# Kernel optimization log

Measured on AMD Instinct MI355X. Metric: run time of the kernel, lower is better.

Reference implementation:

```python
import jax, jax.numpy as jnp
import numpy as np

EMBED_DIM = 512
NUM_HEADS = 8
HEAD_DIM = EMBED_DIM // NUM_HEADS


def setup_inputs() -> dict:
    key = jax.random.key(0)
    ks = jax.random.split(key, 6)
    B, S, E = 2, 4096, EMBED_DIM
    scale = 1.0 / np.sqrt(E)
    return {
        "rotation_params": jax.random.normal(ks[0], (E, E), jnp.float32) * scale,
        "entangle_params": jax.random.normal(ks[1], (E, E), jnp.float32) * scale,
        "inputs": jax.random.normal(ks[2], (B, S, E), jnp.float32),
        "w_q": jax.random.normal(ks[3], (E, E), jnp.float32) * scale,
        "w_k": jax.random.normal(ks[4], (E, E), jnp.float32) * scale,
        "w_v": jax.random.normal(ks[5], (E, E), jnp.float32) * scale,
    }


def reference(rotation_params, entangle_params, inputs, w_q, w_k, w_v):
    B, S, E = inputs.shape
    H, D = NUM_HEADS, HEAD_DIM
    # torch nn.Linear(x) = x @ W.T ; then extra matmul with rotation/entangle mats
    q = (inputs @ w_q.T) @ rotation_params  # [B,S,E]
    k = (inputs @ w_k.T) @ entangle_params  # [B,S,E]
    v = inputs @ w_v.T                       # [B,S,E]
    # split heads -> [B,H,S,D]
    q = q.reshape(B, S, H, D).transpose(0, 2, 1, 3)
    k = k.reshape(B, S, H, D).transpose(0, 2, 1, 3)
    v = v.reshape(B, S, H, D).transpose(0, 2, 1, 3)
    scores = jnp.einsum("bhqd,bhkd->bhqk", q, k) / jnp.sqrt(jnp.float32(D))
    attn = jax.nn.softmax(scores, axis=-1)  # dropout p=0 (eval) -> identity
    out = jnp.einsum("bhqk,bhkd->bhqd", attn, v)
    return out.transpose(0, 2, 1, 3).reshape(B, S, E)
```

## Files before the change

kernel.cpp:

```cpp
#include <hip/hip_runtime.h>
#include <cstddef>

#define E 512
#define H 8
#define D 64
#define BATCH 2
#define SEQ 4096

typedef __attribute__((ext_vector_type(8))) short bf16x8;
typedef __attribute__((ext_vector_type(4))) float f32x4;

__device__ __forceinline__ ushort f2bf(float f) {
  unsigned u = __builtin_bit_cast(unsigned, f);
  u += 0x7fff + ((u >> 16) & 1);
  return (ushort)(u >> 16);
}
__device__ __forceinline__ float bf2f(ushort h) {
  return __builtin_bit_cast(float, (unsigned)h << 16);
}
__device__ __forceinline__ unsigned pk_bf16(float lo, float hi) {
#if __has_builtin(__builtin_amdgcn_cvt_pk_bf16_f32)
  typedef __attribute__((ext_vector_type(2))) __bf16 bfv2;
  bfv2 r = __builtin_amdgcn_cvt_pk_bf16_f32(lo, hi);
  return __builtin_bit_cast(unsigned, r);
#else
  return (unsigned)f2bf(lo) | ((unsigned)f2bf(hi) << 16);
#endif
}
__device__ __forceinline__ float fexp2(float x) {
#if __has_builtin(__builtin_amdgcn_exp2f)
  return __builtin_amdgcn_exp2f(x);
#else
  return exp2f(x);
#endif
}

__global__ __launch_bounds__(256) void xcast(const float* __restrict__ x,
                                             ushort* __restrict__ xh,
                                             ushort* __restrict__ xl) {
  size_t i = ((size_t)blockIdx.x * 256 + threadIdx.x) * 4;
  float4 v = *(const float4*)&x[i];
  ushort4 h, l;
  h.x = f2bf(v.x); l.x = f2bf(v.x - bf2f(h.x));
  h.y = f2bf(v.y); l.y = f2bf(v.y - bf2f(h.y));
  h.z = f2bf(v.z); l.z = f2bf(v.z - bf2f(h.z));
  h.w = f2bf(v.w); l.w = f2bf(v.w - bf2f(h.w));
  *(ushort4*)&xh[i] = h;
  *(ushort4*)&xl[i] = l;
}

__global__ __launch_bounds__(256) void fold_tiled(
    const float* __restrict__ wq, const float* __restrict__ wk,
    const float* __restrict__ rot, const float* __restrict__ ent,
    ushort* __restrict__ weffbT) {
  const int which = blockIdx.z;
  const float* w = which ? wk : wq;
  const float* r = which ? ent : rot;
  const int k = blockIdx.x * 256 + threadIdx.x;
  const int n0 = blockIdx.y * 8;
  float acc[8] = {};
  for (int j0 = 0; j0 < E; j0 += 16) {
    float wv_[16];
#pragma unroll
    for (int u = 0; u < 16; ++u) wv_[u] = w[(size_t)(j0 + u) * E + k];
#pragma unroll
    for (int u = 0; u < 16; ++u)
#pragma unroll
      for (int t = 0; t < 8; ++t)
        acc[t] += wv_[u] * r[(size_t)(j0 + u) * E + n0 + t];
  }
#pragma unroll
  for (int t = 0; t < 8; ++t)
    weffbT[(size_t)which * E * E + (size_t)(n0 + t) * E + k] = f2bf(acc[t]);
}

__global__ __launch_bounds__(256) void wv_cast(const float* __restrict__ wv,
                                               ushort* __restrict__ dst) {
  size_t i = ((size_t)blockIdx.x * 256 + threadIdx.x) * 4;
  float4 v = *(const float4*)&wv[i];
  ushort4 o;
  o.x = f2bf(v.x); o.y = f2bf(v.y); o.z = f2bf(v.z); o.w = f2bf(v.w);
  *(ushort4*)&dst[i] = o;
}

#define LDA 40

__global__ __launch_bounds__(256) void qkv_fused(
    const ushort* __restrict__ xhg, const ushort* __restrict__ xlg,
    const ushort* __restrict__ weffbT, ushort* __restrict__ qg,
    ushort* __restrict__ kg, ushort* __restrict__ vtg) {
  __shared__ ushort sm[5 * 64 * LDA];
  ushort* Ah = sm;
  ushort* Al = sm + 64 * LDA;
  ushort* Bs = sm + 2 * 64 * LDA;
  ushort* vt_tile = Bs;

  const int head = blockIdx.x;
  const int m0 = blockIdx.y * 64;
  const int tid = threadIdx.x;
  const int wave = tid >> 6, lane = tid & 63;
  const int l15 = lane & 15, quad = lane >> 4;
  const int ar = tid >> 2, ac8 = (tid & 3) * 8;

  const ushort* arow = xhg + (size_t)(m0 + ar) * E + ac8;
  const ushort* lrow = xlg + (size_t)(m0 + ar) * E + ac8;
  const ushort* b0row = weffbT + (size_t)(head * 64 + ar) * E + ac8;

  f32x4 acc[3][4];
#pragma unroll
  for (int w = 0; w < 3; ++w)
#pragma unroll
    for (int nt = 0; nt < 4; ++nt) acc[w][nt] = (f32x4){0.f, 0.f, 0.f, 0.f};

  uint4 pa_h = *(const uint4*)&arow[0];
  uint4 pa_l = *(const uint4*)&lrow[0];
  uint4 pb0 = *(const uint4*)&b0row[0];
  uint4 pb1 = *(const uint4*)&b0row[E * E];
  uint4 pb2 = *(const uint4*)&b0row[2 * E * E];

  for (int k0 = 0; k0 < E; k0 += 32) {
    __syncthreads();
    *(uint4*)&Ah[ar * LDA + ac8] = pa_h;
    *(uint4*)&Al[ar * LDA + ac8] = pa_l;
    *(uint4*)&Bs[0 * 64 * LDA + ar * LDA + ac8] = pb0;
    *(uint4*)&Bs[1 * 64 * LDA + ar * LDA + ac8] = pb1;
    *(uint4*)&Bs[2 * 64 * LDA + ar * LDA + ac8] = pb2;
    __syncthreads();

    const int kn = (k0 + 32 < E) ? k0 + 32 : 0;
    pa_h = *(const uint4*)&arow[kn];
    pa_l = *(const uint4*)&lrow[kn];
    pb0 = *(const uint4*)&b0row[kn];
    pb1 = *(const uint4*)&b0row[E * E + kn];
    pb2 = *(const uint4*)&b0row[2 * E * E + kn];

    bf16x8 ah = *(const bf16x8*)&Ah[(wave * 16 + l15) * LDA + quad * 8];
    bf16x8 al = *(const bf16x8*)&Al[(wave * 16 + l15) * LDA + quad * 8];
#pragma unroll
    for (int w = 0; w < 3; ++w)
#pragma unroll
      for (int nt = 0; nt < 4; ++nt) {
        bf16x8 bf = *(const bf16x8*)&Bs[w * 64 * LDA + (nt * 16 + l15) * LDA +
                                        quad * 8];
        acc[w][nt] =
            __builtin_amdgcn_mfma_f32_16x16x32_bf16(ah, bf, acc[w][nt], 0, 0, 0);
        acc[w][nt] =
            __builtin_amdgcn_mfma_f32_16x16x32_bf16(al, bf, acc[w][nt], 0, 0, 0);
      }
  }

  const int b = m0 >> 12;
  const int s_base = m0 & (SEQ - 1);
  const float QSCALE = 0.125f * 1.44269504f;

#pragma unroll
  for (int w = 0; w < 2; ++w) {
    ushort* dst = (w == 0) ? qg : kg;
    float sc = (w == 0) ? QSCALE : 1.0f;
#pragma unroll
    for (int nt = 0; nt < 4; ++nt)
#pragma unroll
      for (int r = 0; r < 4; ++r) {
        float v = acc[w][nt][r] * sc;
        float vo = __shfl_xor(v, 1);
        if (!(lane & 1)) {
          int s = s_base + wave * 16 + quad * 4 + r;
          size_t ix = ((size_t)(b * H + head) * SEQ + s) * D + nt * 16 + l15;
          *(unsigned*)&dst[ix] = pk_bf16(v, vo);
        }
      }
  }

  __syncthreads();
#pragma unroll
  for (int nt = 0; nt < 4; ++nt) {
    uint2 w2;
    w2.x = pk_bf16(acc[2][nt][0], acc[2][nt][1]);
    w2.y = pk_bf16(acc[2][nt][2], acc[2][nt][3]);
    *(uint2*)&vt_tile[(nt * 16 + l15) * 72 + wave * 16 + quad * 4] = w2;
  }
  __syncthreads();
  {
    int vr = tid >> 2, vs = (tid & 3) * 16;
    uint4 c0 = *(const uint4*)&vt_tile[vr * 72 + vs];
    uint4 c1 = *(const uint4*)&vt_tile[vr * 72 + vs + 8];
    size_t vo = ((size_t)(b * H + head) * D + vr) * SEQ + s_base + vs;
    *(uint4*)&vtg[vo] = c0;
    *(uint4*)&vtg[vo + 8] = c1;
  }
}

#define LDK 72

__global__ __launch_bounds__(512, 4) void attn_mfma(
    const ushort* __restrict__ qg, const ushort* __restrict__ kg,
    const ushort* __restrict__ vtg, float* __restrict__ out) {
  __shared__ ushort Ks[2][64 * LDK];
  __shared__ ushort Vs[2][64 * LDK];
  __shared__ ushort Ps[8 * 32 * LDK];
  __shared__ float lex[128];

  const int qt = blockIdx.x;
  const int bh = blockIdx.y;
  const int tid = threadIdx.x;
  const int wave = tid >> 6;
  const int grp = wave >> 2, wq = wave & 3;
  const int lane = tid & 63;
  const int l15 = lane & 15, quad = lane >> 4;
  const int gtid = tid & 255;

  const ushort* qp = qg + (size_t)bh * SEQ * D;
  const ushort* kp = kg + (size_t)bh * SEQ * D;
  const ushort* vp = vtg + (size_t)bh * D * SEQ;
  ushort* Psw = Ps + wave * 32 * LDK;
  ushort* Ksg = Ks[grp];
  ushort* Vsg = Vs[grp];

  const int qrow0 = qt * 128 + wq * 32;
  bf16x8 qf[2][2];
#pragma unroll
  for (int sub = 0; sub < 2; ++sub)
#pragma unroll
    for (int ks = 0; ks < 2; ++ks)
      qf[sub][ks] = *(const bf16x8*)&qp[(size_t)(qrow0 + sub * 16 + l15) * D +
                                        ks * 32 + quad * 8];

  f32x4 o[2][4];
#pragma unroll
  for (int sub = 0; sub < 2; ++sub)
#pragma unroll
    for (int nt = 0; nt < 4; ++nt) o[sub][nt] = (f32x4){0.f, 0.f, 0.f, 0.f};
  float l_r[2] = {0.f, 0.f};

  const int r0 = gtid >> 3, c0 = (gtid & 7) * 8;
  const int r1 = 32 + r0;

  uint4 pk0 = *(const uint4*)&kp[(size_t)grp * 64 * D + r0 * 64 + c0];
  uint4 pk1 = *(const uint4*)&kp[(size_t)grp * 64 * D + r1 * 64 + c0];
  uint4 pv0 = *(const uint4*)&vp[(size_t)r0 * SEQ + grp * 64 + c0];
  uint4 pv1 = *(const uint4*)&vp[(size_t)r1 * SEQ + grp * 64 + c0];

  for (int it = 0; it < SEQ / 128; ++it) {
    __syncthreads();
    *(uint4*)&Ksg[r0 * LDK + c0] = pk0;
    *(uint4*)&Ksg[r1 * LDK + c0] = pk1;
    *(uint4*)&Vsg[r0 * LDK + c0] = pv0;
    *(uint4*)&Vsg[r1 * LDK + c0] = pv1;
    __syncthreads();

    {
      const int itn = (it + 1 < SEQ / 128) ? it + 1 : it;
      const int ktn = itn * 2 + grp;
      const ushort* ksrc = kp + (size_t)ktn * 64 * D;
      pk0 = *(const uint4*)&ksrc[r0 * 64 + c0];
      pk1 = *(const uint4*)&ksrc[r1 * 64 + c0];
      pv0 = *(const uint4*)&vp[(size_t)r0 * SEQ + ktn * 64 + c0];
      pv1 = *(const uint4*)&vp[(size_t)r1 * SEQ + ktn * 64 + c0];
    }

    f32x4 st[2][4];
#pragma unroll
    for (int sub = 0; sub < 2; ++sub)
#pragma unroll
      for (int knt = 0; knt < 4; ++knt)
        st[sub][knt] = (f32x4){0.f, 0.f, 0.f, 0.f};
#pragma unroll
    for (int knt = 0; knt < 4; ++knt)
#pragma unroll
      for (int ks = 0; ks < 2; ++ks) {
        bf16x8 kf =
            *(const bf16x8*)&Ksg[(knt * 16 + l15) * LDK + ks * 32 + quad * 8];
        st[0][knt] = __builtin_amdgcn_mfma_f32_16x16x32_bf16(
            kf, qf[0][ks], st[0][knt], 0, 0, 0);
        st[1][knt] = __builtin_amdgcn_mfma_f32_16x16x32_bf16(
            kf, qf[1][ks], st[1][knt], 0, 0, 0);
      }

#pragma unroll
    for (int sub = 0; sub < 2; ++sub) {
      float rs = 0.f;
#pragma unroll
      for (int knt = 0; knt < 4; ++knt) {
        float p0 = fexp2(st[sub][knt][0]);
        float p1 = fexp2(st[sub][knt][1]);
        float p2 = fexp2(st[sub][knt][2]);
        float p3 = fexp2(st[sub][knt][3]);
        rs += (p0 + p1) + (p2 + p3);
        uint2 w2;
        w2.x = pk_bf16(p0, p1);
        w2.y = pk_bf16(p2, p3);
        *(uint2*)&Psw[(sub * 16 + l15) * LDK + knt * 16 + quad * 4] = w2;
      }
      l_r[sub] += rs;
    }
    __asm__ volatile("s_waitcnt lgkmcnt(0)" ::: "memory");

    bf16x8 pf[2][2];
#pragma unroll
    for (int sub = 0; sub < 2; ++sub)
#pragma unroll
      for (int ks = 0; ks < 2; ++ks)
        pf[sub][ks] = *(const bf16x8*)&Psw[(sub * 16 + l15) * LDK + ks * 32 +
                                           quad * 8];
#pragma unroll
    for (int nt = 0; nt < 4; ++nt)
#pragma unroll
      for (int ks = 0; ks < 2; ++ks) {
        bf16x8 vf =
            *(const bf16x8*)&Vsg[(nt * 16 + l15) * LDK + ks * 32 + quad * 8];
        o[0][nt] = __builtin_amdgcn_mfma_f32_16x16x32_bf16(pf[0][ks], vf,
                                                           o[0][nt], 0, 0, 0);
        o[1][nt] = __builtin_amdgcn_mfma_f32_16x16x32_bf16(pf[1][ks], vf,
                                                           o[1][nt], 0, 0, 0);
      }
  }

  __syncthreads();
  float lsum[2];
#pragma unroll
  for (int sub = 0; sub < 2; ++sub) {
    float l = l_r[sub];
    l += __shfl_xor(l, 16);
    l += __shfl_xor(l, 32);
    lsum[sub] = l;
  }
  float* Oex = (float*)Ps;
  if (grp == 1) {
#pragma unroll
    for (int sub = 0; sub < 2; ++sub)
#pragma unroll
      for (int nt = 0; nt < 4; ++nt)
#pragma unroll
        for (int r = 0; r < 4; ++r)
          Oex[(wq * 32 + sub * 16 + quad * 4 + r) * 68 + nt * 16 + l15] =
              o[sub][nt][r];
    if (quad == 0) {
      lex[wq * 32 + l15] = lsum[0];
      lex[wq * 32 + 16 + l15] = lsum[1];
    }
  }
  __syncthreads();
  if (grp == 0) {
    const int b = bh >> 3, h = bh & 7;
#pragma unroll
    for (int sub = 0; sub < 2; ++sub) {
      float l = lsum[sub] + lex[wq * 32 + sub * 16 + l15];
      float linv = 1.f / l;
      float inv_r[4];
#pragma unroll
      for (int r = 0; r < 4; ++r) inv_r[r] = __shfl(linv, quad * 4 + r);
#pragma unroll
      for (int nt = 0; nt < 4; ++nt)
#pragma unroll
        for (int r = 0; r < 4; ++r) {
          int row = wq * 32 + sub * 16 + quad * 4 + r;
          float val = o[sub][nt][r] + Oex[row * 68 + nt * 16 + l15];
          int srow = qt * 128 + row;
          out[((size_t)b * SEQ + srow) * E + h * D + nt * 16 + l15] =
              val * inv_r[r];
        }
    }
  }
}

extern "C" void kernel_launch(void* const* d_in, const int* in_sizes, int n_in,
                              void* d_out, int out_size, void* d_ws,
                              size_t ws_size, hipStream_t stream) {
  const float* rot = (const float*)d_in[0];
  const float* ent = (const float*)d_in[1];
  const float* x = (const float*)d_in[2];
  const float* wq = (const float*)d_in[3];
  const float* wk = (const float*)d_in[4];
  const float* wv = (const float*)d_in[5];
  float* out = (float*)d_out;

  const size_t NX = (size_t)BATCH * SEQ * E;
  ushort* weffbT = (ushort*)d_ws;
  ushort* xh = weffbT + 3 * E * E;
  ushort* xl = xh + NX;
  ushort* qg = xl + NX;
  ushort* kg = qg + NX;
  ushort* vtg = kg + NX;

  xcast<<<dim3(NX / 1024), 256, 0, stream>>>(x, xh, xl);
  fold_tiled<<<dim3(E / 256, E / 8, 2), 256, 0, stream>>>(wq, wk, rot, ent,
                                                          weffbT);
  wv_cast<<<dim3(E * E / 1024), 256, 0, stream>>>(wv, weffbT + 2 * E * E);
  qkv_fused<<<dim3(H, BATCH * SEQ / 64), 256, 0, stream>>>(xh, xl, weffbT, qg,
                                                           kg, vtg);
  attn_mfma<<<dim3(SEQ / 128, BATCH * H), 512, 0, stream>>>(qg, kg, vtg, out);
}
```

Measured before the change: 251.9 us.

## Retile QKV projection to 128-row blocks with register-direct weight fragments

The QKV projection kernel now uses 128-row M tiles with 512 threads. Each wave computes a 64x48 output subtile across the concatenated Q/K/V columns. Weight fragments are loaded from global memory straight into MFMA operand registers, so weights no longer pass through shared memory, and only the hi/lo activation tiles are staged in LDS. This raises per-wave A-fragment reuse and cuts LDS traffic and block count. In exchange it needs more accumulator registers, and the weight fragment loads are uncoalesced per lane.

Result: no change. 254.2 us (+0.9%).

```diff
diff --git a/kernel.cpp b/kernel.cpp
--- a/kernel.cpp
+++ b/kernel.cpp
@@ -85,108 +85,133 @@
 
 #define LDA 40
 
-__global__ __launch_bounds__(256) void qkv_fused(
+__global__ __launch_bounds__(512) void qkv_v2(
     const ushort* __restrict__ xhg, const ushort* __restrict__ xlg,
     const ushort* __restrict__ weffbT, ushort* __restrict__ qg,
     ushort* __restrict__ kg, ushort* __restrict__ vtg) {
-  __shared__ ushort sm[5 * 64 * LDA];
+  __shared__ ushort sm[2 * 128 * LDA];
   ushort* Ah = sm;
-  ushort* Al = sm + 64 * LDA;
-  ushort* Bs = sm + 2 * 64 * LDA;
-  ushort* vt_tile = Bs;
+  ushort* Al = sm + 128 * LDA;
 
   const int head = blockIdx.x;
-  const int m0 = blockIdx.y * 64;
+  const int m0 = blockIdx.y * 128;
   const int tid = threadIdx.x;
   const int wave = tid >> 6, lane = tid & 63;
   const int l15 = lane & 15, quad = lane >> 4;
-  const int ar = tid >> 2, ac8 = (tid & 3) * 8;
-
-  const ushort* arow = xhg + (size_t)(m0 + ar) * E + ac8;
-  const ushort* lrow = xlg + (size_t)(m0 + ar) * E + ac8;
-  const ushort* b0row = weffbT + (size_t)(head * 64 + ar) * E + ac8;
-
-  f32x4 acc[3][4];
-#pragma unroll
-  for (int w = 0; w < 3; ++w)
-#pragma unroll
-    for (int nt = 0; nt < 4; ++nt) acc[w][nt] = (f32x4){0.f, 0.f, 0.f, 0.f};
-
-  uint4 pa_h = *(const uint4*)&arow[0];
-  uint4 pa_l = *(const uint4*)&lrow[0];
-  uint4 pb0 = *(const uint4*)&b0row[0];
-  uint4 pb1 = *(const uint4*)&b0row[E * E];
-  uint4 pb2 = *(const uint4*)&b0row[2 * E * E];
+  const int mg = wave >> 2, ng = wave & 3;
+
+  const int arow = tid >> 2, ak8 = (tid & 3) * 8;
+  const ushort* aptr_h = xhg + (size_t)(m0 + arow) * E + ak8;
+  const ushort* aptr_l = xlg + (size_t)(m0 + arow) * E + ak8;
+
+  const ushort* bptr[3];
+#pragma unroll
+  for (int nt = 0; nt < 3; ++nt) {
+    int rb = ng * 48 + nt * 16 + l15;
+    bptr[nt] = weffbT +
+               ((size_t)(rb >> 6) * E + head * 64 + (rb & 63)) * E + quad * 8;
+  }
+
+  f32x4 acc[4][3];
+#pragma unroll
+  for (int ms = 0; ms < 4; ++ms)
+#pragma unroll
+    for (int nt = 0; nt < 3; ++nt) acc[ms][nt] = (f32x4){0.f, 0.f, 0.f, 0.f};
+
+  uint4 pa_h = *(const uint4*)aptr_h;
+  uint4 pa_l = *(const uint4*)aptr_l;
+  bf16x8 bf0 = *(const bf16x8*)(bptr[0]);
+  bf16x8 bf1 = *(const bf16x8*)(bptr[1]);
+  bf16x8 bf2 = *(const bf16x8*)(bptr[2]);
 
   for (int k0 = 0; k0 < E; k0 += 32) {
     __syncthreads();
-    *(uint4*)&Ah[ar * LDA + ac8] = pa_h;
-    *(uint4*)&Al[ar * LDA + ac8] = pa_l;
-    *(uint4*)&Bs[0 * 64 * LDA + ar * LDA + ac8] = pb0;
-    *(uint4*)&Bs[1 * 64 * LDA + ar * LDA + ac8] = pb1;
-    *(uint4*)&Bs[2 * 64 * LDA + ar * LDA + ac8] = pb2;
+    *(uint4*)&Ah[arow * LDA + ak8] = pa_h;
+    *(uint4*)&Al[arow * LDA + ak8] = pa_l;
     __syncthreads();
 
     const int kn = (k0 + 32 < E) ? k0 + 32 : 0;
-    pa_h = *(const uint4*)&arow[kn];
-    pa_l = *(const uint4*)&lrow[kn];
-    pb0 = *(const uint4*)&b0row[kn];
-    pb1 = *(const uint4*)&b0row[E * E + kn];
-    pb2 = *(const uint4*)&b0row[2 * E * E + kn];
-
-    bf16x8 ah = *(const bf16x8*)&Ah[(wave * 16 + l15) * LDA + quad * 8];
-    bf16x8 al = *(const bf16x8*)&Al[(wave * 16 + l15) * LDA + quad * 8];
-#pragma unroll
-    for (int w = 0; w < 3; ++w)
-#pragma unroll
-      for (int nt = 0; nt < 4; ++nt) {
-        bf16x8 bf = *(const bf16x8*)&Bs[w * 64 * LDA + (nt * 16 + l15) * LDA +
-                                        quad * 8];
-        acc[w][nt] =
-            __builtin_amdgcn_mfma_f32_16x16x32_bf16(ah, bf, acc[w][nt], 0, 0, 0);
-        acc[w][nt] =
-            __builtin_amdgcn_mfma_f32_16x16x32_bf16(al, bf, acc[w][nt], 0, 0, 0);
-      }
+    pa_h = *(const uint4*)(aptr_h + kn);
+    pa_l = *(const uint4*)(aptr_l + kn);
+    bf16x8 nb0 = *(const bf16x8*)(bptr[0] + kn);
+    bf16x8 nb1 = *(const bf16x8*)(bptr[1] + kn);
+    bf16x8 nb2 = *(const bf16x8*)(bptr[2] + kn);
+
+    bf16x8 ah[4];
+#pragma unroll
+    for (int ms = 0; ms < 4; ++ms)
+      ah[ms] = *(const bf16x8*)&Ah[(mg * 64 + ms * 16 + l15) * LDA + quad * 8];
+#pragma unroll
+    for (int ms = 0; ms < 4; ++ms) {
+      acc[ms][0] =
+          __builtin_amdgcn_mfma_f32_16x16x32_bf16(ah[ms], bf0, acc[ms][0], 0, 0, 0);
+      acc[ms][1] =
+          __builtin_amdgcn_mfma_f32_16x16x32_bf16(ah[ms], bf1, acc[ms][1], 0, 0, 0);
+      acc[ms][2] =
+          __builtin_amdgcn_mfma_f32_16x16x32_bf16(ah[ms], bf2, acc[ms][2], 0, 0, 0);
+    }
+    bf16x8 al[4];
+#pragma unroll
+    for (int ms = 0; ms < 4; ++ms)
+      al[ms] = *(const bf16x8*)&Al[(mg * 64 + ms * 16 + l15) * LDA + quad * 8];
+#pragma unroll
+    for (int ms = 0; ms < 4; ++ms) {
+      acc[ms][0] =
+          __builtin_amdgcn_mfma_f32_16x16x32_bf16(al[ms], bf0, acc[ms][0], 0, 0, 0);
+      acc[ms][1] =
+          __builtin_amdgcn_mfma_f32_16x16x32_bf16(al[ms], bf1, acc[ms][1], 0, 0, 0);
+      acc[ms][2] =
+          __builtin_amdgcn_mfma_f32_16x16x32_bf16(al[ms], bf2, acc[ms][2], 0, 0, 0);
+    }
+    bf0 = nb0; bf1 = nb1; bf2 = nb2;
   }
 
   const int b = m0 >> 12;
   const int s_base = m0 & (SEQ - 1);
   const float QSCALE = 0.125f * 1.44269504f;
 
-#pragma unroll
-  for (int w = 0; w < 2; ++w) {
-    ushort* dst = (w == 0) ? qg : kg;
-    float sc = (w == 0) ? QSCALE : 1.0f;
-#pragma unroll
-    for (int nt = 0; nt < 4; ++nt)
-#pragma unroll
-      for (int r = 0; r < 4; ++r) {
-        float v = acc[w][nt][r] * sc;
-        float vo = __shfl_xor(v, 1);
-        if (!(lane & 1)) {
-          int s = s_base + wave * 16 + quad * 4 + r;
-          size_t ix = ((size_t)(b * H + head) * SEQ + s) * D + nt * 16 + l15;
-          *(unsigned*)&dst[ix] = pk_bf16(v, vo);
+  __syncthreads();
+  ushort* vt = sm;
+
+#pragma unroll
+  for (int nt = 0; nt < 3; ++nt) {
+    const int cbase = ng * 48 + nt * 16;
+    const int w = cbase >> 6;
+    const int dbase = cbase & 63;
+    if (w < 2) {
+      ushort* dst = (w == 0) ? qg : kg;
+      float sc = (w == 0) ? QSCALE : 1.0f;
+#pragma unroll
+      for (int ms = 0; ms < 4; ++ms)
+#pragma unroll
+        for (int r = 0; r < 4; ++r) {
+          float v = acc[ms][nt][r] * sc;
+          float vo = __shfl_xor(v, 1);
+          if (!(lane & 1)) {
+            int s = s_base + mg * 64 + ms * 16 + quad * 4 + r;
+            size_t ix =
+                ((size_t)(b * H + head) * SEQ + s) * D + dbase + l15;
+            *(unsigned*)&dst[ix] = pk_bf16(v, vo);
+          }
         }
+    } else {
+#pragma unroll
+      for (int ms = 0; ms < 4; ++ms) {
+        uint2 w2;
+        w2.x = pk_bf16(acc[ms][nt][0], acc[ms][nt][1]);
+        w2.y = pk_bf16(acc[ms][nt][2], acc[ms][nt][3]);
+        *(uint2*)&vt[(dbase + l15) * 136 + mg * 64 + ms * 16 + quad * 4] = w2;
       }
-  }
-
-  __syncthreads();
-#pragma unroll
-  for (int nt = 0; nt < 4; ++nt) {
-    uint2 w2;
-    w2.x = pk_bf16(acc[2][nt][0], acc[2][nt][1]);
-    w2.y = pk_bf16(acc[2][nt][2], acc[2][nt][3]);
-    *(uint2*)&vt_tile[(nt * 16 + l15) * 72 + wave * 16 + quad * 4] = w2;
+    }
   }
   __syncthreads();
   {
-    int vr = tid >> 2, vs = (tid & 3) * 16;
-    uint4 c0 = *(const uint4*)&vt_tile[vr * 72 + vs];
-    uint4 c1 = *(const uint4*)&vt_tile[vr * 72 + vs + 8];
-    size_t vo = ((size_t)(b * H + head) * D + vr) * SEQ + s_base + vs;
-    *(uint4*)&vtg[vo] = c0;
-    *(uint4*)&vtg[vo + 8] = c1;
+    int d = tid >> 3, mseg = (tid & 7) * 16;
+    uint4 c0 = *(const uint4*)&vt[d * 136 + mseg];
+    uint4 c1 = *(const uint4*)&vt[d * 136 + mseg + 8];
+    size_t vo_ = ((size_t)(b * H + head) * D + d) * SEQ + s_base + mseg;
+    *(uint4*)&vtg[vo_] = c0;
+    *(uint4*)&vtg[vo_ + 8] = c1;
   }
 }
 
@@ -386,7 +411,7 @@
   fold_tiled<<<dim3(E / 256, E / 8, 2), 256, 0, stream>>>(wq, wk, rot, ent,
                                                           weffbT);
   wv_cast<<<dim3(E * E / 1024), 256, 0, stream>>>(wv, weffbT + 2 * E * E);
-  qkv_fused<<<dim3(H, BATCH * SEQ / 64), 256, 0, stream>>>(xh, xl, weffbT, qg,
-                                                           kg, vtg);
+  qkv_v2<<<dim3(H, BATCH * SEQ / 128), 512, 0, stream>>>(xh, xl, weffbT, qg,
+                                                         kg, vtg);
   attn_mfma<<<dim3(SEQ / 128, BATCH * H), 512, 0, stream>>>(qg, kg, vtg, out);
 }
```

## Merge prep kernels and retile QKV GEMM to 128x128 with direct global-to-LDS loads

Applied to the files above, without the earlier changes.

Three preprocessing kernels (x split-cast, weight fold, wv cast) are merged into one launch by dispatching on block index. The QKV projection is retiled from 64-row by one-head (192 columns) blocks to 128x128 output tiles with a K step of 64. Each wave now computes a 64x64 subtile, which raises operand reuse per LDS read. Operands are loaded with global_load_lds instead of register staging, and the old register prefetch of the next tile is dropped. The unpadded LDS layout with a 64-element stride may cause bank conflicts on the fragment reads.

After: 281.9 us. 11.9% more time.

```diff
diff --git a/kernel.cpp b/kernel.cpp
--- a/kernel.cpp
+++ b/kernel.cpp
@@ -34,159 +34,179 @@
   return exp2f(x);
 #endif
 }
-
-__global__ __launch_bounds__(256) void xcast(const float* __restrict__ x,
-                                             ushort* __restrict__ xh,
-                                             ushort* __restrict__ xl) {
-  size_t i = ((size_t)blockIdx.x * 256 + threadIdx.x) * 4;
-  float4 v = *(const float4*)&x[i];
-  ushort4 h, l;
-  h.x = f2bf(v.x); l.x = f2bf(v.x - bf2f(h.x));
-  h.y = f2bf(v.y); l.y = f2bf(v.y - bf2f(h.y));
-  h.z = f2bf(v.z); l.z = f2bf(v.z - bf2f(h.z));
-  h.w = f2bf(v.w); l.w = f2bf(v.w - bf2f(h.w));
-  *(ushort4*)&xh[i] = h;
-  *(ushort4*)&xl[i] = l;
-}
-
-__global__ __launch_bounds__(256) void fold_tiled(
-    const float* __restrict__ wq, const float* __restrict__ wk,
+__device__ __forceinline__ void gl_lds16(const ushort* g, ushort* lds) {
+  __builtin_amdgcn_global_load_lds(
+      (const __attribute__((address_space(1))) unsigned*)g,
+      (__attribute__((address_space(3))) unsigned*)lds, 16, 0, 0);
+}
+
+__global__ __launch_bounds__(256) void prep(
+    const float* __restrict__ x, ushort* __restrict__ xh,
+    ushort* __restrict__ xl, const float* __restrict__ wq,
+    const float* __restrict__ wk, const float* __restrict__ wv,
     const float* __restrict__ rot, const float* __restrict__ ent,
     ushort* __restrict__ weffbT) {
-  const int which = blockIdx.z;
-  const float* w = which ? wk : wq;
-  const float* r = which ? ent : rot;
-  const int k = blockIdx.x * 256 + threadIdx.x;
-  const int n0 = blockIdx.y * 8;
-  float acc[8] = {};
-  for (int j0 = 0; j0 < E; j0 += 16) {
-    float wv_[16];
-#pragma unroll
-    for (int u = 0; u < 16; ++u) wv_[u] = w[(size_t)(j0 + u) * E + k];
-#pragma unroll
-    for (int u = 0; u < 16; ++u)
-#pragma unroll
-      for (int t = 0; t < 8; ++t)
-        acc[t] += wv_[u] * r[(size_t)(j0 + u) * E + n0 + t];
-  }
-#pragma unroll
-  for (int t = 0; t < 8; ++t)
-    weffbT[(size_t)which * E * E + (size_t)(n0 + t) * E + k] = f2bf(acc[t]);
-}
-
-__global__ __launch_bounds__(256) void wv_cast(const float* __restrict__ wv,
-                                               ushort* __restrict__ dst) {
-  size_t i = ((size_t)blockIdx.x * 256 + threadIdx.x) * 4;
-  float4 v = *(const float4*)&wv[i];
-  ushort4 o;
-  o.x = f2bf(v.x); o.y = f2bf(v.y); o.z = f2bf(v.z); o.w = f2bf(v.w);
-  *(ushort4*)&dst[i] = o;
-}
-
-#define LDA 40
-
-__global__ __launch_bounds__(256) void qkv_fused(
+  const int bid = blockIdx.x;
+  const int tid = threadIdx.x;
+  if (bid < 4096) {
+    size_t i = ((size_t)bid * 256 + tid) * 4;
+    float4 v = *(const float4*)&x[i];
+    ushort4 h, l;
+    h.x = f2bf(v.x); l.x = f2bf(v.x - bf2f(h.x));
+    h.y = f2bf(v.y); l.y = f2bf(v.y - bf2f(h.y));
+    h.z = f2bf(v.z); l.z = f2bf(v.z - bf2f(h.z));
+    h.w = f2bf(v.w); l.w = f2bf(v.w - bf2f(h.w));
+    *(ushort4*)&xh[i] = h;
+    *(ushort4*)&xl[i] = l;
+  } else if (bid < 4352) {
+    const int idx = bid - 4096;
+    const int which = idx >> 7;
+    const int n0 = ((idx >> 1) & 63) * 8;
+    const int k = (idx & 1) * 256 + tid;
+    const float* w = which ? wk : wq;
+    const float* r = which ? ent : rot;
+    float acc[8] = {};
+    for (int j0 = 0; j0 < E; j0 += 16) {
+      float wv_[16];
+#pragma unroll
+      for (int u = 0; u < 16; ++u) wv_[u] = w[(size_t)(j0 + u) * E + k];
+#pragma unroll
+      for (int u = 0; u < 16; ++u)
+#pragma unroll
+        for (int t = 0; t < 8; ++t)
+          acc[t] += wv_[u] * r[(size_t)(j0 + u) * E + n0 + t];
+    }
+#pragma unroll
+    for (int t = 0; t < 8; ++t)
+      weffbT[(size_t)which * E * E + (size_t)(n0 + t) * E + k] = f2bf(acc[t]);
+  } else {
+    size_t i = ((size_t)(bid - 4352) * 256 + tid) * 4;
+    float4 v = *(const float4*)&wv[i];
+    ushort4 o;
+    o.x = f2bf(v.x); o.y = f2bf(v.y); o.z = f2bf(v.z); o.w = f2bf(v.w);
+    *(ushort4*)&weffbT[2 * E * E + i] = o;
+  }
+}
+
+__global__ __launch_bounds__(256) void qkv_v3(
     const ushort* __restrict__ xhg, const ushort* __restrict__ xlg,
     const ushort* __restrict__ weffbT, ushort* __restrict__ qg,
     ushort* __restrict__ kg, ushort* __restrict__ vtg) {
-  __shared__ ushort sm[5 * 64 * LDA];
+  __shared__ ushort sm[3 * 128 * 64];
   ushort* Ah = sm;
-  ushort* Al = sm + 64 * LDA;
-  ushort* Bs = sm + 2 * 64 * LDA;
-  ushort* vt_tile = Bs;
-
-  const int head = blockIdx.x;
-  const int m0 = blockIdx.y * 64;
+  ushort* Al = sm + 128 * 64;
+  ushort* Bs = sm + 2 * 128 * 64;
+
+  const int mb = blockIdx.x;
+  const int nb = blockIdx.y;
+  const int m0 = mb * 128;
   const int tid = threadIdx.x;
   const int wave = tid >> 6, lane = tid & 63;
   const int l15 = lane & 15, quad = lane >> 4;
-  const int ar = tid >> 2, ac8 = (tid & 3) * 8;
-
-  const ushort* arow = xhg + (size_t)(m0 + ar) * E + ac8;
-  const ushort* lrow = xlg + (size_t)(m0 + ar) * E + ac8;
-  const ushort* b0row = weffbT + (size_t)(head * 64 + ar) * E + ac8;
-
-  f32x4 acc[3][4];
-#pragma unroll
-  for (int w = 0; w < 3; ++w)
-#pragma unroll
-    for (int nt = 0; nt < 4; ++nt) acc[w][nt] = (f32x4){0.f, 0.f, 0.f, 0.f};
-
-  uint4 pa_h = *(const uint4*)&arow[0];
-  uint4 pa_l = *(const uint4*)&lrow[0];
-  uint4 pb0 = *(const uint4*)&b0row[0];
-  uint4 pb1 = *(const uint4*)&b0row[E * E];
-  uint4 pb2 = *(const uint4*)&b0row[2 * E * E];
-
-  for (int k0 = 0; k0 < E; k0 += 32) {
-    __syncthreads();
-    *(uint4*)&Ah[ar * LDA + ac8] = pa_h;
-    *(uint4*)&Al[ar * LDA + ac8] = pa_l;
-    *(uint4*)&Bs[0 * 64 * LDA + ar * LDA + ac8] = pb0;
-    *(uint4*)&Bs[1 * 64 * LDA + ar * LDA + ac8] = pb1;
-    *(uint4*)&Bs[2 * 64 * LDA + ar * LDA + ac8] = pb2;
-    __syncthreads();
-
-    const int kn = (k0 + 32 < E) ? k0 + 32 : 0;
-    pa_h = *(const uint4*)&arow[kn];
-    pa_l = *(const uint4*)&lrow[kn];
-    pb0 = *(const uint4*)&b0row[kn];
-    pb1 = *(const uint4*)&b0row[E * E + kn];
-    pb2 = *(const uint4*)&b0row[2 * E * E + kn];
-
-    bf16x8 ah = *(const bf16x8*)&Ah[(wave * 16 + l15) * LDA + quad * 8];
-    bf16x8 al = *(const bf16x8*)&Al[(wave * 16 + l15) * LDA + quad * 8];
-#pragma unroll
-    for (int w = 0; w < 3; ++w)
-#pragma unroll
-      for (int nt = 0; nt < 4; ++nt) {
-        bf16x8 bf = *(const bf16x8*)&Bs[w * 64 * LDA + (nt * 16 + l15) * LDA +
-                                        quad * 8];
-        acc[w][nt] =
-            __builtin_amdgcn_mfma_f32_16x16x32_bf16(ah, bf, acc[w][nt], 0, 0, 0);
-        acc[w][nt] =
-            __builtin_amdgcn_mfma_f32_16x16x32_bf16(al, bf, acc[w][nt], 0, 0, 0);
-      }
-  }
-
+  const int wm = (wave >> 1) * 64, wn = (wave & 1) * 64;
+
+  const int srow = wave * 32 + (lane >> 3);
+  const int sch = (lane & 7) * 8;
+  const ushort* gA = xhg + (size_t)(m0 + srow) * E + sch;
+  const ushort* gL = xlg + (size_t)(m0 + srow) * E + sch;
+  const ushort* gB = weffbT + (size_t)(nb * 128 + srow) * E + sch;
+  ushort* sA = Ah + (wave * 32) * 64;
+  ushort* sL = Al + (wave * 32) * 64;
+  ushort* sB = Bs + (wave * 32) * 64;
+
+  f32x4 acc[4][4];
+#pragma unroll
+  for (int ms = 0; ms < 4; ++ms)
+#pragma unroll
+    for (int ns = 0; ns < 4; ++ns) acc[ms][ns] = (f32x4){0.f, 0.f, 0.f, 0.f};
+
+  for (int k0 = 0; k0 < E; k0 += 64) {
+    __syncthreads();
+#pragma unroll
+    for (int i = 0; i < 4; ++i) {
+      gl_lds16(gA + (size_t)(i * 8) * E + k0, sA + i * 8 * 64);
+      gl_lds16(gL + (size_t)(i * 8) * E + k0, sL + i * 8 * 64);
+      gl_lds16(gB + (size_t)(i * 8) * E + k0, sB + i * 8 * 64);
+    }
+    __syncthreads();
+
+#pragma unroll
+    for (int ks = 0; ks < 2; ++ks) {
+      bf16x8 bf[4], ah[4], al[4];
+#pragma unroll
+      for (int ns = 0; ns < 4; ++ns)
+        bf[ns] = *(const bf16x8*)&Bs[(wn + ns * 16 + l15) * 64 + ks * 32 +
+                                     quad * 8];
+#pragma unroll
+      for (int ms = 0; ms < 4; ++ms)
+        ah[ms] = *(const bf16x8*)&Ah[(wm + ms * 16 + l15) * 64 + ks * 32 +
+                                     quad * 8];
+#pragma unroll
+      for (int ms = 0; ms < 4; ++ms)
+#pragma unroll
+        for (int ns = 0; ns < 4; ++ns)
+          acc[ms][ns] = __builtin_amdgcn_mfma_f32_16x16x32_bf16(
+              ah[ms], bf[ns], acc[ms][ns], 0, 0, 0);
+#pragma unroll
+      for (int ms = 0; ms < 4; ++ms)
+        al[ms] = *(const bf16x8*)&Al[(wm + ms * 16 + l15) * 64 + ks * 32 +
+                                     quad * 8];
+#pragma unroll
+      for (int ms = 0; ms < 4; ++ms)
+#pragma unroll
+        for (int ns = 0; ns < 4; ++ns)
+          acc[ms][ns] = __builtin_amdgcn_mfma_f32_16x16x32_bf16(
+              al[ms], bf[ns], acc[ms][ns], 0, 0, 0);
+    }
+  }
+
+  const int wsel = nb >> 2;
+  const int head = (nb & 3) * 2 + (wave & 1);
   const int b = m0 >> 12;
   const int s_base = m0 & (SEQ - 1);
   const float QSCALE = 0.125f * 1.44269504f;
 
-#pragma unroll
-  for (int w = 0; w < 2; ++w) {
-    ushort* dst = (w == 0) ? qg : kg;
-    float sc = (w == 0) ? QSCALE : 1.0f;
-#pragma unroll
-    for (int nt = 0; nt < 4; ++nt)
-#pragma unroll
-      for (int r = 0; r < 4; ++r) {
-        float v = acc[w][nt][r] * sc;
-        float vo = __shfl_xor(v, 1);
-        if (!(lane & 1)) {
-          int s = s_base + wave * 16 + quad * 4 + r;
-          size_t ix = ((size_t)(b * H + head) * SEQ + s) * D + nt * 16 + l15;
-          *(unsigned*)&dst[ix] = pk_bf16(v, vo);
+  if (wsel < 2) {
+    ushort* dst = (wsel == 0) ? qg : kg;
+    const float sc = (wsel == 0) ? QSCALE : 1.0f;
+#pragma unroll
+    for (int ms = 0; ms < 4; ++ms)
+#pragma unroll
+      for (int ns = 0; ns < 4; ++ns)
+#pragma unroll
+        for (int r = 0; r < 4; ++r) {
+          float v = acc[ms][ns][r] * sc;
+          float vo = __shfl_xor(v, 1);
+          if (!(lane & 1)) {
+            int s = s_base + wm + ms * 16 + quad * 4 + r;
+            size_t ix =
+                ((size_t)(b * H + head) * SEQ + s) * D + ns * 16 + l15;
+            *(unsigned*)&dst[ix] = pk_bf16(v, vo);
+          }
         }
+  } else {
+    __syncthreads();
+    ushort* vt = sm;
+#pragma unroll
+    for (int ms = 0; ms < 4; ++ms)
+#pragma unroll
+      for (int ns = 0; ns < 4; ++ns) {
+        uint2 w2;
+        w2.x = pk_bf16(acc[ms][ns][0], acc[ms][ns][1]);
+        w2.y = pk_bf16(acc[ms][ns][2], acc[ms][ns][3]);
+        *(uint2*)&vt[((wave & 1) * 64 + ns * 16 + l15) * 136 + wm + ms * 16 +
+                     quad * 4] = w2;
       }
-  }
-
-  __syncthreads();
-#pragma unroll
-  for (int nt = 0; nt < 4; ++nt) {
-    uint2 w2;
-    w2.x = pk_bf16(acc[2][nt][0], acc[2][nt][1]);
-    w2.y = pk_bf16(acc[2][nt][2], acc[2][nt][3]);
-    *(uint2*)&vt_tile[(nt * 16 + l15) * 72 + wave * 16 + quad * 4] = w2;
-  }
-  __syncthreads();
-  {
-    int vr = tid >> 2, vs = (tid & 3) * 16;
-    uint4 c0 = *(const uint4*)&vt_tile[vr * 72 + vs];
-    uint4 c1 = *(const uint4*)&vt_tile[vr * 72 + vs + 8];
-    size_t vo = ((size_t)(b * H + head) * D + vr) * SEQ + s_base + vs;
-    *(uint4*)&vtg[vo] = c0;
-    *(uint4*)&vtg[vo + 8] = c1;
+    __syncthreads();
+    {
+      int hh = tid >> 7, d = (tid >> 1) & 63, mseg = (tid & 1) * 64;
+      int hd = (nb & 3) * 2 + hh;
+      size_t vo_ = ((size_t)(b * H + hd) * D + d) * SEQ + s_base + mseg;
+      const ushort* src = &vt[(hh * 64 + d) * 136 + mseg];
+#pragma unroll
+      for (int c = 0; c < 8; ++c)
+        *(uint4*)&vtg[vo_ + c * 8] = *(const uint4*)&src[c * 8];
+    }
   }
 }
 
@@ -382,11 +402,8 @@
   ushort* kg = qg + NX;
   ushort* vtg = kg + NX;
 
-  xcast<<<dim3(NX / 1024), 256, 0, stream>>>(x, xh, xl);
-  fold_tiled<<<dim3(E / 256, E / 8, 2), 256, 0, stream>>>(wq, wk, rot, ent,
-                                                          weffbT);
-  wv_cast<<<dim3(E * E / 1024), 256, 0, stream>>>(wv, weffbT + 2 * E * E);
-  qkv_fused<<<dim3(H, BATCH * SEQ / 64), 256, 0, stream>>>(xh, xl, weffbT, qg,
-                                                           kg, vtg);
+  prep<<<dim3(4608), 256, 0, stream>>>(x, xh, xl, wq, wk, wv, rot, ent,
+                                       weffbT);
+  qkv_v3<<<dim3(64, 12), 256, 0, stream>>>(xh, xl, weffbT, qg, kg, vtg);
   attn_mfma<<<dim3(SEQ / 128, BATCH * H), 512, 0, stream>>>(qg, kg, vtg, out);
 }
```
